# Kernel optimization log

Hardware: AMD Instinct MI355X
Metric: run time of the kernel (lower is better)

The kernel has to match this reference:

```python
import jax, jax.numpy as jnp
import numpy as np

B, S, D = 2, 2048, 1024
H, HD = 16, 64          # num_heads, head_dim
W = 16                  # window_size; band half-width = W // 2 = 8


def setup_inputs() -> dict:
    key = jax.random.key(0)
    ks = jax.random.split(key, 5)
    std = 0.02
    inp = {
        'hidden_states': jax.random.normal(ks[0], (B, S, D), dtype=jnp.float32),
        'Wq': jax.random.normal(ks[1], (D, D), dtype=jnp.float32) * std,
        'Wk': jax.random.normal(ks[2], (D, D), dtype=jnp.float32) * std,
        'Wv': jax.random.normal(ks[3], (D, D), dtype=jnp.float32) * std,
        'Wo': jax.random.normal(ks[4], (D, D), dtype=jnp.float32) * std,
        'bq': jnp.zeros((D,), dtype=jnp.float32),
        'bk': jnp.zeros((D,), dtype=jnp.float32),
        'bv': jnp.zeros((D,), dtype=jnp.float32),
        'bo': jnp.zeros((D,), dtype=jnp.float32),
    }
    return inp


def reference(hidden_states, Wq, bq, Wk, bk, Wv, bv, Wo, bo):
    # Projections (y = x @ W + b)
    q = hidden_states @ Wq + bq   # [B,S,D]
    k = hidden_states @ Wk + bk
    v = hidden_states @ Wv + bv
    # Split heads -> [B,H,S,HD]
    q = q.reshape(B, S, H, HD).transpose(0, 2, 1, 3)
    k = k.reshape(B, S, H, HD).transpose(0, 2, 1, 3)
    v = v.reshape(B, S, H, HD).transpose(0, 2, 1, 3)
    # Band mask: original fills scores for j in [i - W//2, i + W//2]
    idx = jnp.arange(S)
    band = jnp.abs(idx[:, None] - idx[None, :]) <= (W // 2)   # [S,S]
    scores = jnp.einsum('bhsd,bhtd->bhst', q, k) / jnp.sqrt(jnp.float32(HD))
    # Faithful to source: out-of-band entries stay 0.0 (NOT -inf),
    # and softmax runs over the FULL row, so exp(0)=1 contributions remain.
    scores = jnp.where(band[None, None], scores, 0.0)
    attn = jax.nn.softmax(scores, axis=-1)                    # [B,H,S,S]
    ctx = jnp.einsum('bhst,bhtd->bhsd', attn, v)              # [B,H,S,HD]
    ctx = ctx.transpose(0, 2, 1, 3).reshape(B, S, D)
    return ctx @ Wo + bo
```

## Files before the change

kernel.cpp:

```cpp
#include <hip/hip_runtime.h>
#include <hip/hip_bf16.h>
#include <cmath>

#define S_LEN 2048
#define DMODEL 1024
#define NH 16
#define HD_DIM 64

typedef __bf16 bf16;
typedef __bf16 bf16x2 __attribute__((ext_vector_type(2)));
typedef __bf16 bf16x8 __attribute__((ext_vector_type(8)));
typedef float f32x4 __attribute__((ext_vector_type(4)));

__global__ __launch_bounds__(256) void prep_all(const float* __restrict__ x,
                                                const float* __restrict__ Wq,
                                                const float* __restrict__ Wk,
                                                const float* __restrict__ Wv,
                                                const float* __restrict__ Wo,
                                                const float* __restrict__ bq,
                                                const float* __restrict__ bk,
                                                const float* __restrict__ bv,
                                                bf16* __restrict__ xb,
                                                bf16* __restrict__ wtall,
                                                bf16* __restrict__ wot,
                                                float* __restrict__ ball,
                                                float* __restrict__ vsm) {
    __shared__ float tile[64][65];
    const int bid = blockIdx.x;
    const int tid = threadIdx.x;
    if (bid < 2048) {
        int i = (bid * 256 + tid) * 8;
        float4 v0 = *(const float4*)(x + i);
        float4 v1 = *(const float4*)(x + i + 4);
        bf16x8 o;
        o[0] = (bf16)v0.x; o[1] = (bf16)v0.y; o[2] = (bf16)v0.z; o[3] = (bf16)v0.w;
        o[4] = (bf16)v1.x; o[5] = (bf16)v1.y; o[6] = (bf16)v1.z; o[7] = (bf16)v1.w;
        *(bf16x8*)(xb + i) = o;
    } else if (bid < 3072) {
        int t = bid - 2048;
        int z = t >> 8;
        t &= 255;
        const float* W = (z == 0) ? Wq : (z == 1) ? Wk : (z == 2) ? Wv : Wo;
        bf16* Wt = (z == 3) ? wot : wtall + (size_t)z * 1048576;
        int n0 = (t & 15) * 64, k0 = (t >> 4) * 64;
        int tr = tid >> 6, tc = tid & 63;
#pragma unroll
        for (int i = 0; i < 16; ++i) {
            int r = tr + i * 4;
            tile[r][tc] = W[(size_t)(k0 + r) * DMODEL + n0 + tc];
        }
        __syncthreads();
#pragma unroll
        for (int i = 0; i < 16; ++i) {
            int r = tr + i * 4;
            Wt[(size_t)(n0 + r) * DMODEL + k0 + tc] = (bf16)tile[tc][r];
        }
    } else {
        int i = (bid - 3072) * 256 + tid;
        float v = (i < 1024) ? bq[i] : (i < 2048) ? bk[i - 1024] : bv[i - 2048];
        ball[i] = v;
        if (i >= 2048) {
            int c = i - 2048;
            vsm[c]        = 2048.0f * v;
            vsm[1024 + c] = 2048.0f * v;
        }
    }
}

__device__ __forceinline__ void gload_lds16(const void* g, void* l) {
    __builtin_amdgcn_global_load_lds((const __attribute__((address_space(1))) void*)g,
                                     (__attribute__((address_space(3))) void*)l, 16, 0, 0);
}

#define BAR() asm volatile("s_barrier" ::: "memory")
#define VMC(N) asm volatile("s_waitcnt vmcnt(" #N ")" ::: "memory")

#define QST_A(T, I) gload_lds16(aSrc + (size_t)((I) * 64) * KDIM + (T) * 64,           \
                                aDstW + ((T) & 1) * 32768 + (I) * 8192)
#define QST_B(T, J) gload_lds16(bSrc + (size_t)((J) * 64) * KDIM + (T) * 64,           \
                                bDstW + ((T) & 1) * 24576 + (J) * 8192)
#define QRD_A(DST, D, MH) do {                                                         \
    _Pragma("unroll") for (int _m = 0; _m < 4; ++_m) {                                 \
        DST[_m][0] = *(const bf16x8*)(sc + (D) * 32768 + aBase + ((MH) * 4 + _m) * 2048 + ks0); \
        DST[_m][1] = *(const bf16x8*)(sc + (D) * 32768 + aBase + ((MH) * 4 + _m) * 2048 + ks1); \
    }                                                                                  \
} while (0)
#define QRD_B01(DST, D) do {                                                           \
    _Pragma("unroll") for (int _n = 0; _n < 2; ++_n) {                                 \
        DST[_n][0] = *(const bf16x8*)(sc + (D) * 24576 + bBase + _n * 2048 + ks0);     \
        DST[_n][1] = *(const bf16x8*)(sc + (D) * 24576 + bBase + _n * 2048 + ks1);     \
    }                                                                                  \
} while (0)
#define QRD_B2(D) do {                                                                 \
    b2[0] = *(const bf16x8*)(sc + (D) * 24576 + bBase + 2 * 2048 + ks0);               \
    b2[1] = *(const bf16x8*)(sc + (D) * 24576 + bBase + 2 * 2048 + ks1);               \
} while (0)
#define QMF16(AS, BS, MH) do {                                                         \
    __builtin_amdgcn_s_setprio(1);                                                     \
    _Pragma("unroll") for (int _m = 0; _m < 4; ++_m)                                   \
    _Pragma("unroll") for (int _n = 0; _n < 2; ++_n)                                   \
    _Pragma("unroll") for (int _k = 0; _k < 2; ++_k)                                   \
        acc[(MH) * 4 + _m][_n] = __builtin_amdgcn_mfma_f32_16x16x32_bf16(              \
            AS[_m][_k], BS[_n][_k], acc[(MH) * 4 + _m][_n], 0, 0, 0);                  \
    __builtin_amdgcn_s_setprio(0);                                                     \
} while (0)
#define QMF8(AS, MH) do {                                                              \
    __builtin_amdgcn_s_setprio(1);                                                     \
    _Pragma("unroll") for (int _m = 0; _m < 4; ++_m)                                   \
    _Pragma("unroll") for (int _k = 0; _k < 2; ++_k)                                   \
        acc[(MH) * 4 + _m][2] = __builtin_amdgcn_mfma_f32_16x16x32_bf16(               \
            AS[_m][_k], b2[_k], acc[(MH) * 4 + _m][2], 0, 0, 0);                       \
    __builtin_amdgcn_s_setprio(0);                                                     \
} while (0)

template <int KDIM>
__global__ __launch_bounds__(512, 2) void gemm_qkv(const bf16* __restrict__ A,
                                                   const bf16* __restrict__ Bt,
                                                   bf16* __restrict__ C,
                                                   const float* __restrict__ bias,
                                                   float* __restrict__ vsm,
                                                   int N) {
    __shared__ bf16 smem[57344];
    char* sc = (char*)smem;

    const int tid  = threadIdx.x;
    const int wv   = tid >> 6;
    const int lane = tid & 63;
    const int ll   = lane & 15;
    const int kh   = lane >> 4;
    const int wm   = wv >> 2;
    const int wn   = wv & 3;

    const int flat = blockIdx.y * 16 + blockIdx.x;
    const int L    = (flat & 7) * 32 + (flat >> 3);
    const int m0   = (L & 15) * 256;
    const int n0   = (L >> 4) * 192;

    const int swcol = (((tid & 7) ^ ((tid >> 3) & 7)) << 3);
    const bf16* aSrc = A + (size_t)(m0 + (tid >> 3)) * KDIM + swcol;
    const bf16* bSrc = Bt + (size_t)(n0 + (tid >> 3)) * KDIM + swcol;
    char* aDstW = sc + wv * 1024;
    char* bDstW = sc + 65536 + wv * 1024;

    const int aBase = wm * 16384 + ll * 128;
    const int bBase = 65536 + (wn * 48 + ll) * 128;
    const int ks0 = ((kh ^ (ll & 7)) << 4);
    const int ks1 = (((4 | kh) ^ (ll & 7)) << 4);

    f32x4 acc[8][3] = {};
    bf16x8 aX[4][2], aY[4][2], bP[2][2], bQ[2][2], b2[2];

    constexpr int NT = KDIM / 64;

    QST_B(0, 0); QST_B(0, 1); QST_B(0, 2);
    QST_A(0, 0); QST_A(0, 1); QST_A(0, 2); QST_A(0, 3);
    QST_B(1, 0); QST_B(1, 1);
    VMC(2); BAR();
    QRD_A(aX, 0, 0); QRD_B01(bP, 0);
    QST_B(1, 2); QST_A(1, 0);
    BAR();

#pragma unroll 1
    for (int i = 0; i < NT / 2 - 1; ++i) {
        const int t = 2 * i;
         QRD_B2(0);                   QMF16(aX, bP, 0); QST_A(t + 1, 1); QST_A(t + 1, 2); BAR();
         QRD_A(aY, 0, 1);             QMF8(aX, 0);      QST_A(t + 1, 3);                  BAR();
                                      QMF8(aY, 1);      QST_B(t + 2, 0); QST_B(t + 2, 1); VMC(2); BAR();
         QRD_A(aX, 1, 0); QRD_B01(bQ, 1); QMF16(aY, bP, 1); QST_B(t + 2, 2); QST_A(t + 2, 0); BAR();
         QRD_B2(1);                   QMF16(aX, bQ, 0); QST_A(t + 2, 1); QST_A(t + 2, 2); BAR();
         QRD_A(aY, 1, 1);             QMF8(aX, 0);      QST_A(t + 2, 3);                  BAR();
                                      QMF8(aY, 1);      QST_B(t + 3, 0); QST_B(t + 3, 1); VMC(2); BAR();
         QRD_A(aX, 0, 0); QRD_B01(bP, 0); QMF16(aY, bQ, 1); QST_B(t + 3, 2); QST_A(t + 3, 0); BAR();
    }

    {
        const int t = NT - 2;
         QRD_B2(0);                       QMF16(aX, bP, 0); QST_A(t + 1, 1); QST_A(t + 1, 2); BAR();
         QRD_A(aY, 0, 1);                 QMF8(aX, 0);      QST_A(t + 1, 3);                  BAR();
                                          QMF8(aY, 1);      VMC(0); BAR();
         QRD_A(aX, 1, 0); QRD_B01(bQ, 1); QMF16(aY, bP, 1); BAR();
         QRD_B2(1);                       QMF16(aX, bQ, 0); BAR();
         QRD_A(aY, 1, 1);                 QMF8(aX, 0);      BAR();
                                       QMF8(aY, 1);      QMF16(aY, bQ, 1);
    }

#pragma unroll
    for (int nf = 0; nf < 3; ++nf) {
        const int col = n0 + wn * 48 + nf * 16 + ll;
        const float bv_ = bias[col];
#pragma unroll
        for (int mf = 0; mf < 8; ++mf) {
            const int row = m0 + wm * 128 + mf * 16 + kh * 4;
#pragma unroll
            for (int r = 0; r < 4; ++r)
                C[(size_t)(row + r) * N + col] = (bf16)(acc[mf][nf][r] + bv_);
        }
    }

    {
        const int bidx = m0 >> 11;
#pragma unroll
        for (int nf = 0; nf < 3; ++nf) {
            if (n0 + wn * 48 + nf * 16 >= 2048) {
                float p = 0.f;
#pragma unroll
                for (int mf = 0; mf < 8; ++mf)
#pragma unroll
                    for (int r = 0; r < 4; ++r) p += acc[mf][nf][r];
                p += __shfl_xor(p, 16);
                p += __shfl_xor(p, 32);
                if (kh == 0)
                    atomicAdd(vsm + bidx * 1024 + (n0 + wn * 48 + nf * 16 + ll - 2048), p);
            }
        }
    }
}

__global__ __launch_bounds__(256) void gemm_bt(const bf16* __restrict__ A,
                                               const bf16* __restrict__ Bt,
                                               float* __restrict__ C,
                                               const float* __restrict__ bias,
                                               int N, int K) {
    __shared__ bf16 As[128 * 32];
    __shared__ bf16 Bs[128 * 32];
    const int tid  = threadIdx.x;
    const int wave = tid >> 6;
    const int lane = tid & 63;

    const int flat = blockIdx.y * 32 + blockIdx.x;
    const int L    = (flat & 7) * 32 + (flat >> 3);
    const int m0   = (L & 31) * 128;
    const int n0   = (L >> 5) * 128;

    const int wm = (wave >> 1) * 64;
    const int wn = (wave & 1) * 64;
    const int lrow = lane & 15;
    const int kh   = lane >> 4;
    const int srow = lane >> 2;
    const int scol = (lane & 3) * 16;

    f32x4 acc[4][4] = {};

    for (int k0 = 0; k0 < K; k0 += 32) {
#pragma unroll
        for (int half = 0; half < 2; ++half) {
            int rbase = half * 64 + wave * 16;
            const char* ga = (const char*)(A + (size_t)(m0 + rbase + srow) * K + k0) + scol;
            gload_lds16(ga, (char*)As + rbase * 64);
            const char* gb = (const char*)(Bt + (size_t)(n0 + rbase + srow) * K + k0) + scol;
            gload_lds16(gb, (char*)Bs + rbase * 64);
        }
        __syncthreads();
        bf16x8 af[4], bfr[4];
#pragma unroll
        for (int mf = 0; mf < 4; ++mf)
            af[mf] = *(const bf16x8*)&As[(wm + mf * 16 + lrow) * 32 + kh * 8];
#pragma unroll
        for (int nf = 0; nf < 4; ++nf)
            bfr[nf] = *(const bf16x8*)&Bs[(wn + nf * 16 + lrow) * 32 + kh * 8];
#pragma unroll
        for (int mf = 0; mf < 4; ++mf)
#pragma unroll
            for (int nf = 0; nf < 4; ++nf)
                acc[mf][nf] = __builtin_amdgcn_mfma_f32_16x16x32_bf16(af[mf], bfr[nf], acc[mf][nf], 0, 0, 0);
        __syncthreads();
    }

#pragma unroll
    for (int mf = 0; mf < 4; ++mf) {
#pragma unroll
        for (int nf = 0; nf < 4; ++nf) {
            int col = n0 + wn + nf * 16 + lrow;
            float bv_ = bias[col];
#pragma unroll
            for (int r = 0; r < 4; ++r) {
                int row = m0 + wm + mf * 16 + kh * 4 + r;
                C[(size_t)row * N + col] = acc[mf][nf][r] + bv_;
            }
        }
    }
}

__global__ __launch_bounds__(256) void band_attn(const bf16* __restrict__ qkv,
                                                 const float* __restrict__ vsum,
                                                 bf16* __restrict__ ctx) {
    int bid = blockIdx.x;
    int it = bid & 31;
    int h  = (bid >> 5) & 15;
    int b  = bid >> 9;
    const int i0 = it * 64;

    __shared__ bf16 qs[64 * 72];
    __shared__ bf16 ks[80 * 72];
    __shared__ bf16 vs[80 * 72];
    __shared__ float wsc[64 * 19];
    __shared__ float wsum[64];

    int tid = threadIdx.x;

    for (int idx = tid; idx < 64 * 8; idx += 256) {
        int r = idx >> 3, c = idx & 7;
        size_t g = (size_t)(b * S_LEN + i0 + r) * 3072 + h * 64 + c * 8;
        *(int4*)&qs[r * 72 + c * 8] = *(const int4*)&qkv[g];
    }
    for (int idx = tid; idx < 80 * 8; idx += 256) {
        int r = idx >> 3, c = idx & 7;
        int j = i0 - 8 + r;
        int4 kv = {0, 0, 0, 0}, vv = {0, 0, 0, 0};
        if (j >= 0 && j < S_LEN) {
            size_t base = (size_t)(b * S_LEN + j) * 3072 + h * 64 + c * 8;
            kv = *(const int4*)&qkv[base + 1024];
            vv = *(const int4*)&qkv[base + 2048];
        }
        *(int4*)&ks[r * 72 + c * 8] = kv;
        *(int4*)&vs[r * 72 + c * 8] = vv;
    }
    __syncthreads();

    {
        int i = tid >> 2, jg = tid & 3;
        bf16x8 qv[8];
#pragma unroll
        for (int c = 0; c < 8; ++c) qv[c] = *(const bf16x8*)&qs[i * 72 + c * 8];
        for (int jj = jg; jj < 17; jj += 4) {
            int j = i0 + i - 8 + jj;
            float w = 0.f;
            if (j >= 0 && j < S_LEN) {
                float dot = 0.f;
#pragma unroll
                for (int c = 0; c < 8; ++c) {
                    bf16x8 kv = *(const bf16x8*)&ks[(i + jj) * 72 + c * 8];
#pragma unroll
                    for (int e = 0; e < 8; ++e) dot += (float)qv[c][e] * (float)kv[e];
                }
                w = expm1f(dot * 0.125f);
            }
            wsc[i * 19 + jj] = w;
        }
    }
    __syncthreads();
    if (tid < 64) {
        float s = 0.f;
#pragma unroll
        for (int jj = 0; jj < 17; ++jj) s += wsc[tid * 19 + jj];
        wsum[tid] = s + (float)S_LEN;
    }
    __syncthreads();

    {
        int d0 = (tid & 31) * 2, ig = tid >> 5;
        float vb0 = vsum[(b * NH + h) * HD_DIM + d0];
        float vb1 = vsum[(b * NH + h) * HD_DIM + d0 + 1];
        for (int i = ig; i < 64; i += 8) {
            float a0 = vb0, a1 = vb1;
#pragma unroll
            for (int jj = 0; jj < 17; ++jj) {
                float w = wsc[i * 19 + jj];
                bf16x2 pv = *(const bf16x2*)&vs[(i + jj) * 72 + d0];
                a0 += w * (float)pv[0];
                a1 += w * (float)pv[1];
            }
            float inv = 1.0f / wsum[i];
            bf16x2 st;
            st[0] = (bf16)(a0 * inv);
            st[1] = (bf16)(a1 * inv);
            *(bf16x2*)&ctx[(size_t)(b * S_LEN + i0 + i) * 1024 + h * 64 + d0] = st;
        }
    }
}

extern "C" void kernel_launch(void* const* d_in, const int* in_sizes, int n_in,
                              void* d_out, int out_size, void* d_ws, size_t ws_size,
                              hipStream_t stream) {
    const float* x  = (const float*)d_in[0];
    const float* Wq = (const float*)d_in[1];
    const float* Wk = (const float*)d_in[2];
    const float* Wv = (const float*)d_in[3];
    const float* Wo = (const float*)d_in[4];
    const float* bq = (const float*)d_in[5];
    const float* bk = (const float*)d_in[6];
    const float* bv = (const float*)d_in[7];
    const float* bo = (const float*)d_in[8];

    char* ws = (char*)d_ws;
    bf16*  xb    = (bf16*)(ws);
    bf16*  wtall = (bf16*)(ws + 8388608);
    bf16*  wot   = (bf16*)(ws + 14680064);
    float* ball  = (float*)(ws + 16777216);
    bf16*  qkv   = (bf16*)(ws + 16789504);
    bf16*  ctxb  = (bf16*)(ws + 41955328);
    float* vsm   = (float*)(ws + 50343936);

    prep_all<<<3084, 256, 0, stream>>>(x, Wq, Wk, Wv, Wo, bq, bk, bv,
                                       xb, wtall, wot, ball, vsm);

    gemm_qkv<1024><<<dim3(16, 16), 512, 0, stream>>>(xb, wtall, qkv, ball, vsm, 3072);

    band_attn<<<1024, 256, 0, stream>>>(qkv, vsm, ctxb);

    gemm_bt<<<dim3(32, 8), 256, 0, stream>>>(ctxb, wot, (float*)d_out, bo, 1024, 1024);
}
```

Before: 85.33 us.

## Shrink QKV GEMM tile to 128x192 with simple double-buffered loop

Replaces the 256x192 tile QKV GEMM and its hand-interleaved ping-pong schedule with a 128x192 tile, 512 blocks, and a plain double-buffered loop that prefetches the next K-slice and then does all LDS reads and MFMAs. LDS use drops and launch bounds allow 4 blocks per CU, which doubles the grid to fill the 256 CUs more evenly and raise occupancy. The cost is less operand reuse per block and losing the fine-grained overlap of loads and MFMAs, since each iteration now ends with a full vmcnt(0) wait and a barrier.

```diff
diff --git a/kernel.cpp b/kernel.cpp
--- a/kernel.cpp
+++ b/kernel.cpp
@@ -75,52 +75,25 @@
 #define BAR() asm volatile("s_barrier" ::: "memory")
 #define VMC(N) asm volatile("s_waitcnt vmcnt(" #N ")" ::: "memory")
 
-#define QST_A(T, I) gload_lds16(aSrc + (size_t)((I) * 64) * KDIM + (T) * 64,           \
-                                aDstW + ((T) & 1) * 32768 + (I) * 8192)
-#define QST_B(T, J) gload_lds16(bSrc + (size_t)((J) * 64) * KDIM + (T) * 64,           \
-                                bDstW + ((T) & 1) * 24576 + (J) * 8192)
-#define QRD_A(DST, D, MH) do {                                                         \
-    _Pragma("unroll") for (int _m = 0; _m < 4; ++_m) {                                 \
-        DST[_m][0] = *(const bf16x8*)(sc + (D) * 32768 + aBase + ((MH) * 4 + _m) * 2048 + ks0); \
-        DST[_m][1] = *(const bf16x8*)(sc + (D) * 32768 + aBase + ((MH) * 4 + _m) * 2048 + ks1); \
-    }                                                                                  \
+#define QST(T, D) do {                                                                 \
+    gload_lds16(aSrc + (size_t)(T) * 64, aDstW + (D) * 16384);                         \
+    gload_lds16(aSrc + (size_t)64 * KDIM + (size_t)(T) * 64,                           \
+                aDstW + (D) * 16384 + 8192);                                           \
+    gload_lds16(bSrc + (size_t)(T) * 64, bDstW + (D) * 24576);                         \
+    gload_lds16(bSrc + (size_t)64 * KDIM + (size_t)(T) * 64,                           \
+                bDstW + (D) * 24576 + 8192);                                           \
+    gload_lds16(bSrc + (size_t)128 * KDIM + (size_t)(T) * 64,                          \
+                bDstW + (D) * 24576 + 16384);                                          \
 } while (0)
-#define QRD_B01(DST, D) do {                                                           \
-    _Pragma("unroll") for (int _n = 0; _n < 2; ++_n) {                                 \
-        DST[_n][0] = *(const bf16x8*)(sc + (D) * 24576 + bBase + _n * 2048 + ks0);     \
-        DST[_n][1] = *(const bf16x8*)(sc + (D) * 24576 + bBase + _n * 2048 + ks1);     \
-    }                                                                                  \
-} while (0)
-#define QRD_B2(D) do {                                                                 \
-    b2[0] = *(const bf16x8*)(sc + (D) * 24576 + bBase + 2 * 2048 + ks0);               \
-    b2[1] = *(const bf16x8*)(sc + (D) * 24576 + bBase + 2 * 2048 + ks1);               \
-} while (0)
-#define QMF16(AS, BS, MH) do {                                                         \
-    __builtin_amdgcn_s_setprio(1);                                                     \
-    _Pragma("unroll") for (int _m = 0; _m < 4; ++_m)                                   \
-    _Pragma("unroll") for (int _n = 0; _n < 2; ++_n)                                   \
-    _Pragma("unroll") for (int _k = 0; _k < 2; ++_k)                                   \
-        acc[(MH) * 4 + _m][_n] = __builtin_amdgcn_mfma_f32_16x16x32_bf16(              \
-            AS[_m][_k], BS[_n][_k], acc[(MH) * 4 + _m][_n], 0, 0, 0);                  \
-    __builtin_amdgcn_s_setprio(0);                                                     \
-} while (0)
-#define QMF8(AS, MH) do {                                                              \
-    __builtin_amdgcn_s_setprio(1);                                                     \
-    _Pragma("unroll") for (int _m = 0; _m < 4; ++_m)                                   \
-    _Pragma("unroll") for (int _k = 0; _k < 2; ++_k)                                   \
-        acc[(MH) * 4 + _m][2] = __builtin_amdgcn_mfma_f32_16x16x32_bf16(               \
-            AS[_m][_k], b2[_k], acc[(MH) * 4 + _m][2], 0, 0, 0);                       \
-    __builtin_amdgcn_s_setprio(0);                                                     \
-} while (0)
 
 template <int KDIM>
-__global__ __launch_bounds__(512, 2) void gemm_qkv(const bf16* __restrict__ A,
+__global__ __launch_bounds__(512, 4) void gemm_qkv(const bf16* __restrict__ A,
                                                    const bf16* __restrict__ Bt,
                                                    bf16* __restrict__ C,
                                                    const float* __restrict__ bias,
                                                    float* __restrict__ vsm,
                                                    int N) {
-    __shared__ bf16 smem[57344];
+    __shared__ bf16 smem[40960];
     char* sc = (char*)smem;
 
     const int tid  = threadIdx.x;
@@ -131,57 +104,58 @@
     const int wm   = wv >> 2;
     const int wn   = wv & 3;
 
-    const int flat = blockIdx.y * 16 + blockIdx.x;
-    const int L    = (flat & 7) * 32 + (flat >> 3);
-    const int m0   = (L & 15) * 256;
-    const int n0   = (L >> 4) * 192;
+    const int flat = blockIdx.y * 32 + blockIdx.x;
+    const int L    = (flat & 7) * 64 + (flat >> 3);
+    const int m0   = (L & 31) * 128;
+    const int n0   = (L >> 5) * 192;
 
     const int swcol = (((tid & 7) ^ ((tid >> 3) & 7)) << 3);
     const bf16* aSrc = A + (size_t)(m0 + (tid >> 3)) * KDIM + swcol;
     const bf16* bSrc = Bt + (size_t)(n0 + (tid >> 3)) * KDIM + swcol;
     char* aDstW = sc + wv * 1024;
-    char* bDstW = sc + 65536 + wv * 1024;
-
-    const int aBase = wm * 16384 + ll * 128;
-    const int bBase = 65536 + (wn * 48 + ll) * 128;
+    char* bDstW = sc + 32768 + wv * 1024;
+
+    const int aBase = wm * 8192 + ll * 128;
+    const int bBase = (wn * 48 + ll) * 128;
     const int ks0 = ((kh ^ (ll & 7)) << 4);
     const int ks1 = (((4 | kh) ^ (ll & 7)) << 4);
 
-    f32x4 acc[8][3] = {};
-    bf16x8 aX[4][2], aY[4][2], bP[2][2], bQ[2][2], b2[2];
+    f32x4 acc[4][3] = {};
 
     constexpr int NT = KDIM / 64;
 
-    QST_B(0, 0); QST_B(0, 1); QST_B(0, 2);
-    QST_A(0, 0); QST_A(0, 1); QST_A(0, 2); QST_A(0, 3);
-    QST_B(1, 0); QST_B(1, 1);
-    VMC(2); BAR();
-    QRD_A(aX, 0, 0); QRD_B01(bP, 0);
-    QST_B(1, 2); QST_A(1, 0);
-    BAR();
+    QST(0, 0);
+    VMC(0); BAR();
 
 #pragma unroll 1
-    for (int i = 0; i < NT / 2 - 1; ++i) {
-        const int t = 2 * i;
-         QRD_B2(0);                   QMF16(aX, bP, 0); QST_A(t + 1, 1); QST_A(t + 1, 2); BAR();
-         QRD_A(aY, 0, 1);             QMF8(aX, 0);      QST_A(t + 1, 3);                  BAR();
-                                      QMF8(aY, 1);      QST_B(t + 2, 0); QST_B(t + 2, 1); VMC(2); BAR();
-         QRD_A(aX, 1, 0); QRD_B01(bQ, 1); QMF16(aY, bP, 1); QST_B(t + 2, 2); QST_A(t + 2, 0); BAR();
-         QRD_B2(1);                   QMF16(aX, bQ, 0); QST_A(t + 2, 1); QST_A(t + 2, 2); BAR();
-         QRD_A(aY, 1, 1);             QMF8(aX, 0);      QST_A(t + 2, 3);                  BAR();
-                                      QMF8(aY, 1);      QST_B(t + 3, 0); QST_B(t + 3, 1); VMC(2); BAR();
-         QRD_A(aX, 0, 0); QRD_B01(bP, 0); QMF16(aY, bQ, 1); QST_B(t + 3, 2); QST_A(t + 3, 0); BAR();
-    }
-
-    {
-        const int t = NT - 2;
-         QRD_B2(0);                       QMF16(aX, bP, 0); QST_A(t + 1, 1); QST_A(t + 1, 2); BAR();
-         QRD_A(aY, 0, 1);                 QMF8(aX, 0);      QST_A(t + 1, 3);                  BAR();
-                                          QMF8(aY, 1);      VMC(0); BAR();
-         QRD_A(aX, 1, 0); QRD_B01(bQ, 1); QMF16(aY, bP, 1); BAR();
-         QRD_B2(1);                       QMF16(aX, bQ, 0); BAR();
-         QRD_A(aY, 1, 1);                 QMF8(aX, 0);      BAR();
-                                       QMF8(aY, 1);      QMF16(aY, bQ, 1);
+    for (int t = 0; t < NT; ++t) {
+        const int d = t & 1;
+        if (t + 1 < NT) QST(t + 1, d ^ 1);
+
+        bf16x8 a[4][2], b[3][2];
+#pragma unroll
+        for (int mf = 0; mf < 4; ++mf) {
+            a[mf][0] = *(const bf16x8*)(sc + d * 16384 + aBase + mf * 2048 + ks0);
+            a[mf][1] = *(const bf16x8*)(sc + d * 16384 + aBase + mf * 2048 + ks1);
+        }
+#pragma unroll
+        for (int nf = 0; nf < 3; ++nf) {
+            b[nf][0] = *(const bf16x8*)(sc + 32768 + d * 24576 + bBase + nf * 2048 + ks0);
+            b[nf][1] = *(const bf16x8*)(sc + 32768 + d * 24576 + bBase + nf * 2048 + ks1);
+        }
+
+        __builtin_amdgcn_s_setprio(1);
+#pragma unroll
+        for (int mf = 0; mf < 4; ++mf)
+#pragma unroll
+            for (int nf = 0; nf < 3; ++nf)
+#pragma unroll
+                for (int k = 0; k < 2; ++k)
+                    acc[mf][nf] = __builtin_amdgcn_mfma_f32_16x16x32_bf16(
+                        a[mf][k], b[nf][k], acc[mf][nf], 0, 0, 0);
+        __builtin_amdgcn_s_setprio(0);
+
+        VMC(0); BAR();
     }
 
 #pragma unroll
@@ -189,8 +163,8 @@
         const int col = n0 + wn * 48 + nf * 16 + ll;
         const float bv_ = bias[col];
 #pragma unroll
-        for (int mf = 0; mf < 8; ++mf) {
-            const int row = m0 + wm * 128 + mf * 16 + kh * 4;
+        for (int mf = 0; mf < 4; ++mf) {
+            const int row = m0 + wm * 64 + mf * 16 + kh * 4;
 #pragma unroll
             for (int r = 0; r < 4; ++r)
                 C[(size_t)(row + r) * N + col] = (bf16)(acc[mf][nf][r] + bv_);
@@ -204,7 +178,7 @@
             if (n0 + wn * 48 + nf * 16 >= 2048) {
                 float p = 0.f;
 #pragma unroll
-                for (int mf = 0; mf < 8; ++mf)
+                for (int mf = 0; mf < 4; ++mf)
 #pragma unroll
                     for (int r = 0; r < 4; ++r) p += acc[mf][nf][r];
                 p += __shfl_xor(p, 16);
@@ -394,7 +368,7 @@
     prep_all<<<3084, 256, 0, stream>>>(x, Wq, Wk, Wv, Wo, bq, bk, bv,
                                        xb, wtall, wot, ball, vsm);
 
-    gemm_qkv<1024><<<dim3(16, 16), 512, 0, stream>>>(xb, wtall, qkv, ball, vsm, 3072);
+    gemm_qkv<1024><<<dim3(32, 16), 512, 0, stream>>>(xb, wtall, qkv, ball, vsm, 3072);
 
     band_attn<<<1024, 256, 0, stream>>>(qkv, vsm, ctxb);
 
```

New measurement: 83.19 us. 2.5% less time.
